# Performance work log

Measured on AMD Instinct MI355X. Metric: run time of the kernel, lower is better.

The kernel has to match this reference:

```python
import jax, jax.numpy as jnp
import numpy as np

N_EMBD = 768
HEAD_SIZE = 64
B, T = 8, 4096


def setup_inputs() -> dict:
    key = jax.random.key(0)
    ks = jax.random.split(key, 7)
    s = 0.02  # small init scale for weights
    return {
        "x": jax.random.normal(ks[0], (B, T, N_EMBD), dtype=jnp.float32),
        "Wq": jax.random.normal(ks[1], (N_EMBD, HEAD_SIZE), dtype=jnp.float32) * s,
        "bq": jax.random.normal(ks[2], (HEAD_SIZE,), dtype=jnp.float32) * s,
        "Wk": jax.random.normal(ks[3], (N_EMBD, HEAD_SIZE), dtype=jnp.float32) * s,
        "bk": jax.random.normal(ks[4], (HEAD_SIZE,), dtype=jnp.float32) * s,
        "Wv": jax.random.normal(ks[5], (N_EMBD, HEAD_SIZE), dtype=jnp.float32) * s,
        "bv": jax.random.normal(ks[6], (HEAD_SIZE,), dtype=jnp.float32) * s,
    }


def reference(x, Wq, bq, Wk, bk, Wv, bv):
    # x: [B, T, C]; note: scale uses C = n_embd (input dim), per the original code.
    C = x.shape[-1]
    scale = jnp.asarray(C, x.dtype) ** -0.5
    q = x @ Wq + bq  # [B, T, H]
    k = x @ Wk + bk  # [B, T, H]
    v = x @ Wv + bv  # [B, T, H]
    wei = jnp.einsum("bqh,bkh->bqk", q, k) * scale  # [B, T, T]
    att = jax.nn.softmax(wei, axis=-1)
    # dropout p=0.0 (eval mode) -> identity
    out = jnp.einsum("bqk,bkh->bqh", att, v)  # [B, T, H]
    return out
```

## Files before the change

### kernel.cpp

```cpp
#include <hip/hip_runtime.h>
#include <stdint.h>

#define T_SEQ 4096
#define CEMB 768
#define HS 64

typedef __attribute__((ext_vector_type(8))) short bf16x8;
typedef __attribute__((ext_vector_type(16))) float f32x16;
typedef __attribute__((ext_vector_type(4))) unsigned int u32x4;

__device__ __forceinline__ short bfru(float f) {
    uint32_t u = __builtin_bit_cast(uint32_t, f);
    return (short)((u + 0x8000u) >> 16);
}
__device__ __forceinline__ uint32_t cvtpk_bf16(float lo, float hi) {
    uint32_t r;
    asm("v_cvt_pk_bf16_f32 %0, %1, %2" : "=v"(r) : "v"(lo), "v"(hi));
    return r;
}

#define QSCALE (0.036084391824351615f * 1.4426950408889634f)

__global__ __launch_bounds__(256) void prep_wt(const float* __restrict__ Wq,
                                               const float* __restrict__ Wk,
                                               const float* __restrict__ Wv,
                                               short* __restrict__ wtf) {
    const int p = blockIdx.x;
    const int tid = threadIdx.x;
    const int lane = tid & 63, jp = tid >> 6;
    const int l31 = lane & 31, lhi = lane >> 5;
    const int kq = p % 48, ct = p / 48;
    const int k = kq * 16 + lhi * 8 + jp * 2;
    const int nn = ct * 32 + l31;
    const float* W = nn < 64 ? Wq : (nn < 128 ? Wk : Wv);
    const int col = nn & 63;
    uint32_t lo = (uint16_t)bfru(W[k * 64 + col]);
    uint32_t hi = (uint16_t)bfru(W[(k + 1) * 64 + col]);
    *(uint32_t*)&wtf[(p * 64 + lane) * 8 + jp * 2] = lo | (hi << 16);
}

__global__ __launch_bounds__(256, 2) void qkv_proj(const float* __restrict__ x,
        const float* __restrict__ bq, const float* __restrict__ bk, const float* __restrict__ bv,
        const short* __restrict__ wtf,
        short* __restrict__ qo, short* __restrict__ ko, short* __restrict__ vto) {
    __shared__ short S[2][64 * 72];

    const int tid  = threadIdx.x;
    const int wave = tid >> 6, lane = tid & 63;
    const int l31  = lane & 31, lhi = lane >> 5;
    const int rg   = wave & 1;
    const int ctb  = (wave >> 1) * 3;
    const int rowbase = blockIdx.x * 64;

    f32x16 acc[3];
    #pragma unroll
    for (int c = 0; c < 3; ++c) {
        const int ct = ctb + c, nn = ct * 32 + l31;
        const float bb = nn < 64 ? bq[nn] : (nn < 128 ? bk[nn - 64] : bv[nn - 128]);
        #pragma unroll
        for (int r = 0; r < 16; ++r) acc[c][r] = bb;
    }

    const int sr = tid >> 2, sseg = (tid & 3) * 16;
    const float* xrow = x + (long)(rowbase + sr) * CEMB + sseg;
    const short* wfb = wtf + (long)ctb * 48 * 512 + lane * 8;

    float4 RA0, RA1, RA2, RA3;
    float4 RB0, RB1, RB2, RB3;
    {
        const float4* s0 = (const float4*)xrow;
        RA0 = s0[0]; RA1 = s0[1]; RA2 = s0[2]; RA3 = s0[3];
        const float4* s1 = (const float4*)(xrow + 64);
        RB0 = s1[0]; RB1 = s1[1]; RB2 = s1[2]; RB3 = s1[3];
        bf16x8 w0, w1;
        w0[0]=bfru(RA0.x); w0[1]=bfru(RA0.y); w0[2]=bfru(RA0.z); w0[3]=bfru(RA0.w);
        w0[4]=bfru(RA1.x); w0[5]=bfru(RA1.y); w0[6]=bfru(RA1.z); w0[7]=bfru(RA1.w);
        w1[0]=bfru(RA2.x); w1[1]=bfru(RA2.y); w1[2]=bfru(RA2.z); w1[3]=bfru(RA2.w);
        w1[4]=bfru(RA3.x); w1[5]=bfru(RA3.y); w1[6]=bfru(RA3.z); w1[7]=bfru(RA3.w);
        *(bf16x8*)&S[0][sr * 72 + sseg]     = w0;
        *(bf16x8*)&S[0][sr * 72 + sseg + 8] = w1;
    }
    __syncthreads();

    #pragma unroll
    for (int kt = 0; kt < 12; ++kt) {
        const int cur = kt & 1;
        bf16x8 wfr[12];
        #pragma unroll
        for (int kc = 0; kc < 4; ++kc)
            #pragma unroll
            for (int c = 0; c < 3; ++c)
                wfr[kc * 3 + c] = *(const bf16x8*)(wfb + ((c * 48 + kt * 4 + kc) << 9));
        if (kt + 2 < 12) {
            const float4* sn = (const float4*)(xrow + (kt + 2) * 64);
            if (cur == 0) { RA0 = sn[0]; RA1 = sn[1]; RA2 = sn[2]; RA3 = sn[3]; }
            else          { RB0 = sn[0]; RB1 = sn[1]; RB2 = sn[2]; RB3 = sn[3]; }
        }
        #pragma unroll
        for (int kc = 0; kc < 4; ++kc) {
            bf16x8 af = *(const bf16x8*)&S[cur][(rg * 32 + l31) * 72 + kc * 16 + lhi * 8];
            acc[0] = __builtin_amdgcn_mfma_f32_32x32x16_bf16(af, wfr[kc * 3 + 0], acc[0], 0, 0, 0);
            acc[1] = __builtin_amdgcn_mfma_f32_32x32x16_bf16(af, wfr[kc * 3 + 1], acc[1], 0, 0, 0);
            acc[2] = __builtin_amdgcn_mfma_f32_32x32x16_bf16(af, wfr[kc * 3 + 2], acc[2], 0, 0, 0);
        }
        if (kt + 1 < 12) {
            bf16x8 w0, w1;
            if (cur == 0) {
                w0[0]=bfru(RB0.x); w0[1]=bfru(RB0.y); w0[2]=bfru(RB0.z); w0[3]=bfru(RB0.w);
                w0[4]=bfru(RB1.x); w0[5]=bfru(RB1.y); w0[6]=bfru(RB1.z); w0[7]=bfru(RB1.w);
                w1[0]=bfru(RB2.x); w1[1]=bfru(RB2.y); w1[2]=bfru(RB2.z); w1[3]=bfru(RB2.w);
                w1[4]=bfru(RB3.x); w1[5]=bfru(RB3.y); w1[6]=bfru(RB3.z); w1[7]=bfru(RB3.w);
            } else {
                w0[0]=bfru(RA0.x); w0[1]=bfru(RA0.y); w0[2]=bfru(RA0.z); w0[3]=bfru(RA0.w);
                w0[4]=bfru(RA1.x); w0[5]=bfru(RA1.y); w0[6]=bfru(RA1.z); w0[7]=bfru(RA1.w);
                w1[0]=bfru(RA2.x); w1[1]=bfru(RA2.y); w1[2]=bfru(RA2.z); w1[3]=bfru(RA2.w);
                w1[4]=bfru(RA3.x); w1[5]=bfru(RA3.y); w1[6]=bfru(RA3.z); w1[7]=bfru(RA3.w);
            }
            *(bf16x8*)&S[cur ^ 1][sr * 72 + sseg]     = w0;
            *(bf16x8*)&S[cur ^ 1][sr * 72 + sseg + 8] = w1;
        }
        __syncthreads();
    }

    #pragma unroll
    for (int c = 0; c < 3; ++c) {
        const int ct = ctb + c;
        if (ct < 2) {
            #pragma unroll
            for (int r = 0; r < 16; ++r) {
                const int row = rg * 32 + (r & 3) + 8 * (r >> 2) + 4 * lhi;
                qo[(long)(rowbase + row) * HS + ct * 32 + l31] = bfru(acc[c][r] * QSCALE);
            }
        } else if (ct < 4) {
            #pragma unroll
            for (int r = 0; r < 16; ++r) {
                const int row = rg * 32 + (r & 3) + 8 * (r >> 2) + 4 * lhi;
                ko[(long)(rowbase + row) * HS + (ct - 2) * 32 + l31] = bfru(acc[c][r]);
            }
        } else {
            #pragma unroll
            for (int r = 0; r < 16; ++r) {
                const int row = rg * 32 + (r & 3) + 8 * (r >> 2) + 4 * lhi;
                S[0][((ct - 4) * 32 + l31) * 72 + row] = bfru(acc[c][r]);
            }
        }
    }
    __syncthreads();
    if (tid < 128) {
        const int vcol = tid >> 1, hh = tid & 1;
        const int b = rowbase >> 12, t0 = rowbase & 4095;
        short* dst = vto + ((long)b * HS + vcol) * T_SEQ + t0 + hh * 32;
        #pragma unroll
        for (int i = 0; i < 4; ++i)
            *(bf16x8*)(dst + i * 8) = *(const bf16x8*)&S[0][vcol * 72 + hh * 32 + i * 8];
    }
}

__global__ __launch_bounds__(256, 2) void attn(const short* __restrict__ qm,
        const short* __restrict__ km, const short* __restrict__ vtm,
        float* __restrict__ Op, float* __restrict__ lp, const int ks,
        float* __restrict__ outdirect) {
    __shared__ short Klds[2][64 * 72];
    __shared__ short Vlds[2][64 * 72];
    __shared__ float Lred[4][2][32];

    const int tid  = threadIdx.x;
    const int wave = tid >> 6, lane = tid & 63;
    const int l31  = lane & 31, lhi = lane >> 5;
    const int idx  = blockIdx.x;
    const int b = idx & 7, s = (idx >> 3) % ks, qt = idx / (8 * ks);
    const int slab = T_SEQ / ks, nkt = slab / 64;

    const short* qb = qm + ((long)b * T_SEQ + qt * 256 + wave * 64) * HS;
    const short* kb = km + ((long)b * T_SEQ + s * slab) * HS;
    const short* vb = vtm + (long)b * HS * T_SEQ + s * slab;

    bf16x8 qf[2][4];
    #pragma unroll
    for (int qs = 0; qs < 2; ++qs)
        #pragma unroll
        for (int kc = 0; kc < 4; ++kc)
            qf[qs][kc] = *(const bf16x8*)&qb[(qs * 32 + l31) * HS + kc * 16 + lhi * 8];

    f32x16 oacc[2][2] = {};
    float lsum[2] = {0.f, 0.f};

    const int sr = tid >> 2, sc = (tid & 3) * 16;
    const short* kp = kb + sr * HS + sc;
    const short* vp = vb + sr * T_SEQ + sc;

    bf16x8 kr0 = *(const bf16x8*)kp, kr1 = *(const bf16x8*)(kp + 8);
    bf16x8 vr0 = *(const bf16x8*)vp, vr1 = *(const bf16x8*)(vp + 8);
    *(bf16x8*)&Klds[0][sr * 72 + sc]     = kr0;
    *(bf16x8*)&Klds[0][sr * 72 + sc + 8] = kr1;
    *(bf16x8*)&Vlds[0][sr * 72 + sc]     = vr0;
    *(bf16x8*)&Vlds[0][sr * 72 + sc + 8] = vr1;
    __syncthreads();

    for (int kt = 0; kt < nkt; ++kt) {
        const int cur = kt & 1;
        const bool pfe = (kt + 1 < nkt);
        if (pfe) {
            const short* kp2 = kp + (kt + 1) * (64 * HS);
            const short* vp2 = vp + (kt + 1) * 64;
            kr0 = *(const bf16x8*)kp2; kr1 = *(const bf16x8*)(kp2 + 8);
            vr0 = *(const bf16x8*)vp2; vr1 = *(const bf16x8*)(vp2 + 8);
        }
        const short* Kc = Klds[cur];
        const short* Vc = Vlds[cur];
        #pragma unroll
        for (int ct = 0; ct < 2; ++ct) {
            const short* krow = &Kc[(ct * 32 + l31) * 72 + lhi * 8];
            bf16x8 kf0 = *(const bf16x8*)(krow);
            bf16x8 kf1 = *(const bf16x8*)(krow + 16);
            bf16x8 kf2 = *(const bf16x8*)(krow + 32);
            bf16x8 kf3 = *(const bf16x8*)(krow + 48);
            const short* vrow = &Vc[l31 * 72 + ct * 32 + lhi * 8];
            bf16x8 vf00 = *(const bf16x8*)(vrow);
            bf16x8 vf10 = *(const bf16x8*)(vrow + 16);
            bf16x8 vf01 = *(const bf16x8*)(vrow + 32 * 72);
            bf16x8 vf11 = *(const bf16x8*)(vrow + 32 * 72 + 16);
            #pragma unroll
            for (int qs = 0; qs < 2; ++qs) {
                f32x16 z = {};
                z = __builtin_amdgcn_mfma_f32_32x32x16_bf16(kf0, qf[qs][0], z, 0, 0, 0);
                z = __builtin_amdgcn_mfma_f32_32x32x16_bf16(kf1, qf[qs][1], z, 0, 0, 0);
                z = __builtin_amdgcn_mfma_f32_32x32x16_bf16(kf2, qf[qs][2], z, 0, 0, 0);
                z = __builtin_amdgcn_mfma_f32_32x32x16_bf16(kf3, qf[qs][3], z, 0, 0, 0);
                #pragma unroll
                for (int r = 0; r < 16; ++r) z[r] = __builtin_amdgcn_exp2f(z[r]);
                lsum[qs] += (((z[0]+z[1])+(z[2]+z[3])) + ((z[4]+z[5])+(z[6]+z[7])))
                          + (((z[8]+z[9])+(z[10]+z[11])) + ((z[12]+z[13])+(z[14]+z[15])));
                uint32_t x0 = cvtpk_bf16(z[0],  z[1]),  y0 = cvtpk_bf16(z[4],  z[5]);
                uint32_t x1 = cvtpk_bf16(z[2],  z[3]),  y1 = cvtpk_bf16(z[6],  z[7]);
                uint32_t x2 = cvtpk_bf16(z[8],  z[9]),  y2 = cvtpk_bf16(z[12], z[13]);
                uint32_t x3 = cvtpk_bf16(z[10], z[11]), y3 = cvtpk_bf16(z[14], z[15]);
                asm("v_permlane32_swap_b32 %0, %1" : "+v"(x0), "+v"(y0));
                asm("v_permlane32_swap_b32 %0, %1" : "+v"(x1), "+v"(y1));
                asm("v_permlane32_swap_b32 %0, %1" : "+v"(x2), "+v"(y2));
                asm("v_permlane32_swap_b32 %0, %1" : "+v"(x3), "+v"(y3));
                u32x4 t0 = {x0, x1, y0, y1};
                u32x4 t1 = {x2, x3, y2, y3};
                bf16x8 pa0 = __builtin_bit_cast(bf16x8, t0);
                bf16x8 pa1 = __builtin_bit_cast(bf16x8, t1);
                oacc[qs][0] = __builtin_amdgcn_mfma_f32_32x32x16_bf16(pa0, vf00, oacc[qs][0], 0, 0, 0);
                oacc[qs][1] = __builtin_amdgcn_mfma_f32_32x32x16_bf16(pa0, vf01, oacc[qs][1], 0, 0, 0);
                oacc[qs][0] = __builtin_amdgcn_mfma_f32_32x32x16_bf16(pa1, vf10, oacc[qs][0], 0, 0, 0);
                oacc[qs][1] = __builtin_amdgcn_mfma_f32_32x32x16_bf16(pa1, vf11, oacc[qs][1], 0, 0, 0);
            }
        }
        if (pfe) {
            const int nxt = cur ^ 1;
            *(bf16x8*)&Klds[nxt][sr * 72 + sc]     = kr0;
            *(bf16x8*)&Klds[nxt][sr * 72 + sc + 8] = kr1;
            *(bf16x8*)&Vlds[nxt][sr * 72 + sc]     = vr0;
            *(bf16x8*)&Vlds[nxt][sr * 72 + sc + 8] = vr1;
        }
        __syncthreads();
    }

    #pragma unroll
    for (int qs = 0; qs < 2; ++qs) lsum[qs] += __shfl_xor(lsum[qs], 32);

    const long rowg = (long)b * T_SEQ + qt * 256 + wave * 64;
    if (outdirect) {
        if (lhi == 0) { Lred[wave][0][l31] = lsum[0]; Lred[wave][1][l31] = lsum[1]; }
        __syncthreads();
        float* ob = outdirect + rowg * HS;
        #pragma unroll
        for (int qs = 0; qs < 2; ++qs)
            #pragma unroll
            for (int ht = 0; ht < 2; ++ht)
                #pragma unroll
                for (int r = 0; r < 16; ++r) {
                    const int row = (r & 3) + 8 * (r >> 2) + 4 * lhi;
                    ob[(long)(qs * 32 + row) * HS + ht * 32 + l31] =
                        oacc[qs][ht][r] / Lred[wave][qs][row];
                }
    } else {
        float* op = Op + ((long)s * 32768 + rowg) * HS;
        #pragma unroll
        for (int qs = 0; qs < 2; ++qs)
            #pragma unroll
            for (int ht = 0; ht < 2; ++ht)
                #pragma unroll
                for (int r = 0; r < 16; ++r) {
                    const int row = (r & 3) + 8 * (r >> 2) + 4 * lhi;
                    op[(qs * 32 + row) * HS + ht * 32 + l31] = oacc[qs][ht][r];
                }
        if (lhi == 0) {
            lp[(long)s * 32768 + rowg + l31]      = lsum[0];
            lp[(long)s * 32768 + rowg + 32 + l31] = lsum[1];
        }
    }
}

__global__ __launch_bounds__(256) void combine(const float4* __restrict__ Op,
        const float* __restrict__ lp, float4* __restrict__ out, const int ks) {
    const int idx = blockIdx.x * 256 + threadIdx.x;
    const int row = idx >> 4, h4 = idx & 15;
    float ox = 0.f, oy = 0.f, oz = 0.f, ow = 0.f, l = 0.f;
    for (int s = 0; s < ks; ++s) {
        float4 t = Op[(long)(s * 32768 + row) * 16 + h4];
        ox += t.x; oy += t.y; oz += t.z; ow += t.w;
        l += lp[s * 32768 + row];
    }
    const float inv = 1.0f / l;
    float4 o; o.x = ox * inv; o.y = oy * inv; o.z = oz * inv; o.w = ow * inv;
    out[(long)row * 16 + h4] = o;
}

extern "C" void kernel_launch(void* const* d_in, const int* in_sizes, int n_in,
                              void* d_out, int out_size, void* d_ws, size_t ws_size,
                              hipStream_t stream) {
    const float* x  = (const float*)d_in[0];
    const float* Wq = (const float*)d_in[1];
    const float* bq = (const float*)d_in[2];
    const float* Wk = (const float*)d_in[3];
    const float* bk = (const float*)d_in[4];
    const float* Wv = (const float*)d_in[5];
    const float* bv = (const float*)d_in[6];

    char* ws = (char*)d_ws;
    short* qo  = (short*)(ws);
    short* ko  = (short*)(ws + (4u << 20));
    short* vto = (short*)(ws + (8u << 20));
    short* wtf = (short*)(ws + (12u << 20));
    const size_t opOff = 12582912u + 294912u;
    float* Op = (float*)(ws + opOff);

    const size_t per_s = 8388608u + 131072u;
    int ks = (ws_size >= opOff + 4 * per_s) ? 4
           : (ws_size >= opOff + 2 * per_s) ? 2 : 1;
    float* lp = (float*)(ws + opOff + (size_t)ks * 8388608u);

    prep_wt<<<288, 256, 0, stream>>>(Wq, Wk, Wv, wtf);
    qkv_proj<<<512, 256, 0, stream>>>(x, bq, bk, bv, wtf, qo, ko, vto);
    attn<<<128 * ks, 256, 0, stream>>>(qo, ko, vto, Op, lp, ks,
                                       ks == 1 ? (float*)d_out : nullptr);
    if (ks > 1)
        combine<<<2048, 256, 0, stream>>>((const float4*)Op, lp, (float4*)d_out, ks);
}
```

Before: 216.2 us.

## Fuse weight prep, QKV projection, attention and combine into one persistent kernel

Replaces four separate kernel launches with a single 512-block kernel whose stages are separated by software grid barriers built on atomic counters in workspace, which are zeroed by a memset before each launch. The aim is to remove launch gaps and per-kernel tail effects between the small stages. The risks are deadlock if all 512 blocks cannot be co-resident, the cost of spinning on global atomics, and the grid being fixed at 512 blocks, which leaves blocks idle in stages that need fewer.

After: 398.6 us. 1.84x slower.

```diff
diff --git a/kernel.cpp b/kernel.cpp
--- a/kernel.cpp
+++ b/kernel.cpp
@@ -4,6 +4,7 @@
 #define T_SEQ 4096
 #define CEMB 768
 #define HS 64
+#define GRIDN 512u
 
 typedef __attribute__((ext_vector_type(8))) short bf16x8;
 typedef __attribute__((ext_vector_type(16))) float f32x16;
@@ -21,293 +22,315 @@
 
 #define QSCALE (0.036084391824351615f * 1.4426950408889634f)
 
-__global__ __launch_bounds__(256) void prep_wt(const float* __restrict__ Wq,
-                                               const float* __restrict__ Wk,
-                                               const float* __restrict__ Wv,
-                                               short* __restrict__ wtf) {
-    const int p = blockIdx.x;
-    const int tid = threadIdx.x;
-    const int lane = tid & 63, jp = tid >> 6;
-    const int l31 = lane & 31, lhi = lane >> 5;
-    const int kq = p % 48, ct = p / 48;
-    const int k = kq * 16 + lhi * 8 + jp * 2;
-    const int nn = ct * 32 + l31;
-    const float* W = nn < 64 ? Wq : (nn < 128 ? Wk : Wv);
-    const int col = nn & 63;
-    uint32_t lo = (uint16_t)bfru(W[k * 64 + col]);
-    uint32_t hi = (uint16_t)bfru(W[(k + 1) * 64 + col]);
-    *(uint32_t*)&wtf[(p * 64 + lane) * 8 + jp * 2] = lo | (hi << 16);
-}
-
-__global__ __launch_bounds__(256, 2) void qkv_proj(const float* __restrict__ x,
-        const float* __restrict__ bq, const float* __restrict__ bk, const float* __restrict__ bv,
-        const short* __restrict__ wtf,
-        short* __restrict__ qo, short* __restrict__ ko, short* __restrict__ vto) {
-    __shared__ short S[2][64 * 72];
+__device__ __forceinline__ void gridbar(unsigned* c) {
+    __syncthreads();
+    if (threadIdx.x == 0) {
+        __hip_atomic_fetch_add(c, 1u, __ATOMIC_RELEASE, __HIP_MEMORY_SCOPE_AGENT);
+        while (__hip_atomic_load(c, __ATOMIC_ACQUIRE, __HIP_MEMORY_SCOPE_AGENT) < GRIDN)
+            __builtin_amdgcn_s_sleep(2);
+    }
+    __syncthreads();
+}
+
+__global__ __launch_bounds__(256, 2) void fused(
+        const float* __restrict__ x,
+        const float* __restrict__ Wq, const float* __restrict__ bq,
+        const float* __restrict__ Wk, const float* __restrict__ bk,
+        const float* __restrict__ Wv, const float* __restrict__ bv,
+        short* __restrict__ qo, short* __restrict__ ko, short* __restrict__ vto,
+        short* __restrict__ wtf, float* __restrict__ Op, float* __restrict__ lp,
+        unsigned* bars, const int ks, float* __restrict__ outf) {
+    __shared__ __align__(16) char smem[37888];
 
     const int tid  = threadIdx.x;
+    const int bid  = blockIdx.x;
     const int wave = tid >> 6, lane = tid & 63;
     const int l31  = lane & 31, lhi = lane >> 5;
-    const int rg   = wave & 1;
-    const int ctb  = (wave >> 1) * 3;
-    const int rowbase = blockIdx.x * 64;
-
-    f32x16 acc[3];
-    #pragma unroll
-    for (int c = 0; c < 3; ++c) {
-        const int ct = ctb + c, nn = ct * 32 + l31;
-        const float bb = nn < 64 ? bq[nn] : (nn < 128 ? bk[nn - 64] : bv[nn - 128]);
-        #pragma unroll
-        for (int r = 0; r < 16; ++r) acc[c][r] = bb;
-    }
-
-    const int sr = tid >> 2, sseg = (tid & 3) * 16;
-    const float* xrow = x + (long)(rowbase + sr) * CEMB + sseg;
-    const short* wfb = wtf + (long)ctb * 48 * 512 + lane * 8;
-
-    float4 RA0, RA1, RA2, RA3;
-    float4 RB0, RB1, RB2, RB3;
+
+    if (bid < 288) {
+        const int p = bid;
+        const int jp = wave;
+        const int kq = p % 48, ct = p / 48;
+        const int k = kq * 16 + lhi * 8 + jp * 2;
+        const int nn = ct * 32 + l31;
+        const float* W = nn < 64 ? Wq : (nn < 128 ? Wk : Wv);
+        const int col = nn & 63;
+        uint32_t lo = (uint16_t)bfru(W[k * 64 + col]);
+        uint32_t hi = (uint16_t)bfru(W[(k + 1) * 64 + col]);
+        *(uint32_t*)&wtf[(p * 64 + lane) * 8 + jp * 2] = lo | (hi << 16);
+    }
+    gridbar(bars + 0);
+
     {
-        const float4* s0 = (const float4*)xrow;
-        RA0 = s0[0]; RA1 = s0[1]; RA2 = s0[2]; RA3 = s0[3];
-        const float4* s1 = (const float4*)(xrow + 64);
-        RB0 = s1[0]; RB1 = s1[1]; RB2 = s1[2]; RB3 = s1[3];
-        bf16x8 w0, w1;
-        w0[0]=bfru(RA0.x); w0[1]=bfru(RA0.y); w0[2]=bfru(RA0.z); w0[3]=bfru(RA0.w);
-        w0[4]=bfru(RA1.x); w0[5]=bfru(RA1.y); w0[6]=bfru(RA1.z); w0[7]=bfru(RA1.w);
-        w1[0]=bfru(RA2.x); w1[1]=bfru(RA2.y); w1[2]=bfru(RA2.z); w1[3]=bfru(RA2.w);
-        w1[4]=bfru(RA3.x); w1[5]=bfru(RA3.y); w1[6]=bfru(RA3.z); w1[7]=bfru(RA3.w);
-        *(bf16x8*)&S[0][sr * 72 + sseg]     = w0;
-        *(bf16x8*)&S[0][sr * 72 + sseg + 8] = w1;
-    }
-    __syncthreads();
-
-    #pragma unroll
-    for (int kt = 0; kt < 12; ++kt) {
-        const int cur = kt & 1;
-        bf16x8 wfr[12];
-        #pragma unroll
-        for (int kc = 0; kc < 4; ++kc)
-            #pragma unroll
-            for (int c = 0; c < 3; ++c)
-                wfr[kc * 3 + c] = *(const bf16x8*)(wfb + ((c * 48 + kt * 4 + kc) << 9));
-        if (kt + 2 < 12) {
-            const float4* sn = (const float4*)(xrow + (kt + 2) * 64);
-            if (cur == 0) { RA0 = sn[0]; RA1 = sn[1]; RA2 = sn[2]; RA3 = sn[3]; }
-            else          { RB0 = sn[0]; RB1 = sn[1]; RB2 = sn[2]; RB3 = sn[3]; }
-        }
-        #pragma unroll
-        for (int kc = 0; kc < 4; ++kc) {
-            bf16x8 af = *(const bf16x8*)&S[cur][(rg * 32 + l31) * 72 + kc * 16 + lhi * 8];
-            acc[0] = __builtin_amdgcn_mfma_f32_32x32x16_bf16(af, wfr[kc * 3 + 0], acc[0], 0, 0, 0);
-            acc[1] = __builtin_amdgcn_mfma_f32_32x32x16_bf16(af, wfr[kc * 3 + 1], acc[1], 0, 0, 0);
-            acc[2] = __builtin_amdgcn_mfma_f32_32x32x16_bf16(af, wfr[kc * 3 + 2], acc[2], 0, 0, 0);
-        }
-        if (kt + 1 < 12) {
+        short* S0 = (short*)smem;
+        short* S1 = (short*)(smem + 9216);
+        const int rg   = wave & 1;
+        const int ctb  = (wave >> 1) * 3;
+        const int rowbase = bid * 64;
+
+        f32x16 acc[3];
+        #pragma unroll
+        for (int c = 0; c < 3; ++c) {
+            const int ct = ctb + c, nn = ct * 32 + l31;
+            const float bb = nn < 64 ? bq[nn] : (nn < 128 ? bk[nn - 64] : bv[nn - 128]);
+            #pragma unroll
+            for (int r = 0; r < 16; ++r) acc[c][r] = bb;
+        }
+
+        const int sr = tid >> 2, sseg = (tid & 3) * 16;
+        const float* xrow = x + (long)(rowbase + sr) * CEMB + sseg;
+        const short* wfb = wtf + (long)ctb * 48 * 512 + lane * 8;
+
+        float4 RA0, RA1, RA2, RA3;
+        float4 RB0, RB1, RB2, RB3;
+        {
+            const float4* s0 = (const float4*)xrow;
+            RA0 = s0[0]; RA1 = s0[1]; RA2 = s0[2]; RA3 = s0[3];
+            const float4* s1 = (const float4*)(xrow + 64);
+            RB0 = s1[0]; RB1 = s1[1]; RB2 = s1[2]; RB3 = s1[3];
             bf16x8 w0, w1;
-            if (cur == 0) {
-                w0[0]=bfru(RB0.x); w0[1]=bfru(RB0.y); w0[2]=bfru(RB0.z); w0[3]=bfru(RB0.w);
-                w0[4]=bfru(RB1.x); w0[5]=bfru(RB1.y); w0[6]=bfru(RB1.z); w0[7]=bfru(RB1.w);
-                w1[0]=bfru(RB2.x); w1[1]=bfru(RB2.y); w1[2]=bfru(RB2.z); w1[3]=bfru(RB2.w);
-                w1[4]=bfru(RB3.x); w1[5]=bfru(RB3.y); w1[6]=bfru(RB3.z); w1[7]=bfru(RB3.w);
+            w0[0]=bfru(RA0.x); w0[1]=bfru(RA0.y); w0[2]=bfru(RA0.z); w0[3]=bfru(RA0.w);
+            w0[4]=bfru(RA1.x); w0[5]=bfru(RA1.y); w0[6]=bfru(RA1.z); w0[7]=bfru(RA1.w);
+            w1[0]=bfru(RA2.x); w1[1]=bfru(RA2.y); w1[2]=bfru(RA2.z); w1[3]=bfru(RA2.w);
+            w1[4]=bfru(RA3.x); w1[5]=bfru(RA3.y); w1[6]=bfru(RA3.z); w1[7]=bfru(RA3.w);
+            *(bf16x8*)&S0[sr * 72 + sseg]     = w0;
+            *(bf16x8*)&S0[sr * 72 + sseg + 8] = w1;
+        }
+        __syncthreads();
+
+        #pragma unroll
+        for (int kt = 0; kt < 12; ++kt) {
+            const int cur = kt & 1;
+            short* Sc = cur ? S1 : S0;
+            short* Sn = cur ? S0 : S1;
+            bf16x8 wfr[12];
+            #pragma unroll
+            for (int kc = 0; kc < 4; ++kc)
+                #pragma unroll
+                for (int c = 0; c < 3; ++c)
+                    wfr[kc * 3 + c] = *(const bf16x8*)(wfb + ((c * 48 + kt * 4 + kc) << 9));
+            if (kt + 2 < 12) {
+                const float4* sn = (const float4*)(xrow + (kt + 2) * 64);
+                if (cur == 0) { RA0 = sn[0]; RA1 = sn[1]; RA2 = sn[2]; RA3 = sn[3]; }
+                else          { RB0 = sn[0]; RB1 = sn[1]; RB2 = sn[2]; RB3 = sn[3]; }
+            }
+            #pragma unroll
+            for (int kc = 0; kc < 4; ++kc) {
+                bf16x8 af = *(const bf16x8*)&Sc[(rg * 32 + l31) * 72 + kc * 16 + lhi * 8];
+                acc[0] = __builtin_amdgcn_mfma_f32_32x32x16_bf16(af, wfr[kc * 3 + 0], acc[0], 0, 0, 0);
+                acc[1] = __builtin_amdgcn_mfma_f32_32x32x16_bf16(af, wfr[kc * 3 + 1], acc[1], 0, 0, 0);
+                acc[2] = __builtin_amdgcn_mfma_f32_32x32x16_bf16(af, wfr[kc * 3 + 2], acc[2], 0, 0, 0);
+            }
+            if (kt + 1 < 12) {
+                bf16x8 w0, w1;
+                if (cur == 0) {
+                    w0[0]=bfru(RB0.x); w0[1]=bfru(RB0.y); w0[2]=bfru(RB0.z); w0[3]=bfru(RB0.w);
+                    w0[4]=bfru(RB1.x); w0[5]=bfru(RB1.y); w0[6]=bfru(RB1.z); w0[7]=bfru(RB1.w);
+                    w1[0]=bfru(RB2.x); w1[1]=bfru(RB2.y); w1[2]=bfru(RB2.z); w1[3]=bfru(RB2.w);
+                    w1[4]=bfru(RB3.x); w1[5]=bfru(RB3.y); w1[6]=bfru(RB3.z); w1[7]=bfru(RB3.w);
+                } else {
+                    w0[0]=bfru(RA0.x); w0[1]=bfru(RA0.y); w0[2]=bfru(RA0.z); w0[3]=bfru(RA0.w);
+                    w0[4]=bfru(RA1.x); w0[5]=bfru(RA1.y); w0[6]=bfru(RA1.z); w0[7]=bfru(RA1.w);
+                    w1[0]=bfru(RA2.x); w1[1]=bfru(RA2.y); w1[2]=bfru(RA2.z); w1[3]=bfru(RA2.w);
+                    w1[4]=bfru(RA3.x); w1[5]=bfru(RA3.y); w1[6]=bfru(RA3.z); w1[7]=bfru(RA3.w);
+                }
+                *(bf16x8*)&Sn[sr * 72 + sseg]     = w0;
+                *(bf16x8*)&Sn[sr * 72 + sseg + 8] = w1;
+            }
+            __syncthreads();
+        }
+
+        #pragma unroll
+        for (int c = 0; c < 3; ++c) {
+            const int ct = ctb + c;
+            if (ct < 2) {
+                #pragma unroll
+                for (int r = 0; r < 16; ++r) {
+                    const int row = rg * 32 + (r & 3) + 8 * (r >> 2) + 4 * lhi;
+                    qo[(long)(rowbase + row) * HS + ct * 32 + l31] = bfru(acc[c][r] * QSCALE);
+                }
+            } else if (ct < 4) {
+                #pragma unroll
+                for (int r = 0; r < 16; ++r) {
+                    const int row = rg * 32 + (r & 3) + 8 * (r >> 2) + 4 * lhi;
+                    ko[(long)(rowbase + row) * HS + (ct - 2) * 32 + l31] = bfru(acc[c][r]);
+                }
             } else {
-                w0[0]=bfru(RA0.x); w0[1]=bfru(RA0.y); w0[2]=bfru(RA0.z); w0[3]=bfru(RA0.w);
-                w0[4]=bfru(RA1.x); w0[5]=bfru(RA1.y); w0[6]=bfru(RA1.z); w0[7]=bfru(RA1.w);
-                w1[0]=bfru(RA2.x); w1[1]=bfru(RA2.y); w1[2]=bfru(RA2.z); w1[3]=bfru(RA2.w);
-                w1[4]=bfru(RA3.x); w1[5]=bfru(RA3.y); w1[6]=bfru(RA3.z); w1[7]=bfru(RA3.w);
-            }
-            *(bf16x8*)&S[cur ^ 1][sr * 72 + sseg]     = w0;
-            *(bf16x8*)&S[cur ^ 1][sr * 72 + sseg + 8] = w1;
+                #pragma unroll
+                for (int r = 0; r < 16; ++r) {
+                    const int row = rg * 32 + (r & 3) + 8 * (r >> 2) + 4 * lhi;
+                    S0[((ct - 4) * 32 + l31) * 72 + row] = bfru(acc[c][r]);
+                }
+            }
         }
         __syncthreads();
-    }
-
-    #pragma unroll
-    for (int c = 0; c < 3; ++c) {
-        const int ct = ctb + c;
-        if (ct < 2) {
-            #pragma unroll
-            for (int r = 0; r < 16; ++r) {
-                const int row = rg * 32 + (r & 3) + 8 * (r >> 2) + 4 * lhi;
-                qo[(long)(rowbase + row) * HS + ct * 32 + l31] = bfru(acc[c][r] * QSCALE);
-            }
-        } else if (ct < 4) {
-            #pragma unroll
-            for (int r = 0; r < 16; ++r) {
-                const int row = rg * 32 + (r & 3) + 8 * (r >> 2) + 4 * lhi;
-                ko[(long)(rowbase + row) * HS + (ct - 2) * 32 + l31] = bfru(acc[c][r]);
-            }
+        if (tid < 128) {
+            const int vcol = tid >> 1, hh = tid & 1;
+            const int b = rowbase >> 12, t0 = rowbase & 4095;
+            short* dst = vto + ((long)b * HS + vcol) * T_SEQ + t0 + hh * 32;
+            #pragma unroll
+            for (int i = 0; i < 4; ++i)
+                *(bf16x8*)(dst + i * 8) = *(const bf16x8*)&S0[vcol * 72 + hh * 32 + i * 8];
+        }
+    }
+    gridbar(bars + 1);
+
+    if (bid < 128 * ks) {
+        short* KldsB = (short*)smem;
+        short* VldsB = (short*)(smem + 18432);
+        float* LredB = (float*)(smem + 36864);
+
+        const int idx = bid;
+        const int b = idx & 7, s = (idx >> 3) % ks, qt = idx / (8 * ks);
+        const int slab = T_SEQ / ks, nkt = slab / 64;
+
+        const short* qb = qo + ((long)b * T_SEQ + qt * 256 + wave * 64) * HS;
+        const short* kb = ko + ((long)b * T_SEQ + s * slab) * HS;
+        const short* vb = vto + (long)b * HS * T_SEQ + s * slab;
+
+        bf16x8 qf[2][4];
+        #pragma unroll
+        for (int qs = 0; qs < 2; ++qs)
+            #pragma unroll
+            for (int kc = 0; kc < 4; ++kc)
+                qf[qs][kc] = *(const bf16x8*)&qb[(qs * 32 + l31) * HS + kc * 16 + lhi * 8];
+
+        f32x16 oacc[2][2] = {};
+        float lsum[2] = {0.f, 0.f};
+
+        const int sr = tid >> 2, sc = (tid & 3) * 16;
+        const short* kp = kb + sr * HS + sc;
+        const short* vp = vb + sr * T_SEQ + sc;
+
+        bf16x8 kr0 = *(const bf16x8*)kp, kr1 = *(const bf16x8*)(kp + 8);
+        bf16x8 vr0 = *(const bf16x8*)vp, vr1 = *(const bf16x8*)(vp + 8);
+        *(bf16x8*)&KldsB[sr * 72 + sc]     = kr0;
+        *(bf16x8*)&KldsB[sr * 72 + sc + 8] = kr1;
+        *(bf16x8*)&VldsB[sr * 72 + sc]     = vr0;
+        *(bf16x8*)&VldsB[sr * 72 + sc + 8] = vr1;
+        __syncthreads();
+
+        for (int kt = 0; kt < nkt; ++kt) {
+            const int cur = kt & 1;
+            const bool pfe = (kt + 1 < nkt);
+            if (pfe) {
+                const short* kp2 = kp + (kt + 1) * (64 * HS);
+                const short* vp2 = vp + (kt + 1) * 64;
+                kr0 = *(const bf16x8*)kp2; kr1 = *(const bf16x8*)(kp2 + 8);
+                vr0 = *(const bf16x8*)vp2; vr1 = *(const bf16x8*)(vp2 + 8);
+            }
+            const short* Kc = KldsB + cur * 4608;
+            const short* Vc = VldsB + cur * 4608;
+            #pragma unroll
+            for (int ct = 0; ct < 2; ++ct) {
+                const short* krow = &Kc[(ct * 32 + l31) * 72 + lhi * 8];
+                bf16x8 kf0 = *(const bf16x8*)(krow);
+                bf16x8 kf1 = *(const bf16x8*)(krow + 16);
+                bf16x8 kf2 = *(const bf16x8*)(krow + 32);
+                bf16x8 kf3 = *(const bf16x8*)(krow + 48);
+                const short* vrow = &Vc[l31 * 72 + ct * 32 + lhi * 8];
+                bf16x8 vf00 = *(const bf16x8*)(vrow);
+                bf16x8 vf10 = *(const bf16x8*)(vrow + 16);
+                bf16x8 vf01 = *(const bf16x8*)(vrow + 32 * 72);
+                bf16x8 vf11 = *(const bf16x8*)(vrow + 32 * 72 + 16);
+                #pragma unroll
+                for (int qs = 0; qs < 2; ++qs) {
+                    f32x16 z = {};
+                    z = __builtin_amdgcn_mfma_f32_32x32x16_bf16(kf0, qf[qs][0], z, 0, 0, 0);
+                    z = __builtin_amdgcn_mfma_f32_32x32x16_bf16(kf1, qf[qs][1], z, 0, 0, 0);
+                    z = __builtin_amdgcn_mfma_f32_32x32x16_bf16(kf2, qf[qs][2], z, 0, 0, 0);
+                    z = __builtin_amdgcn_mfma_f32_32x32x16_bf16(kf3, qf[qs][3], z, 0, 0, 0);
+                    #pragma unroll
+                    for (int r = 0; r < 16; ++r) z[r] = __builtin_amdgcn_exp2f(z[r]);
+                    lsum[qs] += (((z[0]+z[1])+(z[2]+z[3])) + ((z[4]+z[5])+(z[6]+z[7])))
+                              + (((z[8]+z[9])+(z[10]+z[11])) + ((z[12]+z[13])+(z[14]+z[15])));
+                    uint32_t x0 = cvtpk_bf16(z[0],  z[1]),  y0 = cvtpk_bf16(z[4],  z[5]);
+                    uint32_t x1 = cvtpk_bf16(z[2],  z[3]),  y1 = cvtpk_bf16(z[6],  z[7]);
+                    uint32_t x2 = cvtpk_bf16(z[8],  z[9]),  y2 = cvtpk_bf16(z[12], z[13]);
+                    uint32_t x3 = cvtpk_bf16(z[10], z[11]), y3 = cvtpk_bf16(z[14], z[15]);
+                    asm("v_permlane32_swap_b32 %0, %1" : "+v"(x0), "+v"(y0));
+                    asm("v_permlane32_swap_b32 %0, %1" : "+v"(x1), "+v"(y1));
+                    asm("v_permlane32_swap_b32 %0, %1" : "+v"(x2), "+v"(y2));
+                    asm("v_permlane32_swap_b32 %0, %1" : "+v"(x3), "+v"(y3));
+                    u32x4 t0 = {x0, x1, y0, y1};
+                    u32x4 t1 = {x2, x3, y2, y3};
+                    bf16x8 pa0 = __builtin_bit_cast(bf16x8, t0);
+                    bf16x8 pa1 = __builtin_bit_cast(bf16x8, t1);
+                    oacc[qs][0] = __builtin_amdgcn_mfma_f32_32x32x16_bf16(pa0, vf00, oacc[qs][0], 0, 0, 0);
+                    oacc[qs][1] = __builtin_amdgcn_mfma_f32_32x32x16_bf16(pa0, vf01, oacc[qs][1], 0, 0, 0);
+                    oacc[qs][0] = __builtin_amdgcn_mfma_f32_32x32x16_bf16(pa1, vf10, oacc[qs][0], 0, 0, 0);
+                    oacc[qs][1] = __builtin_amdgcn_mfma_f32_32x32x16_bf16(pa1, vf11, oacc[qs][1], 0, 0, 0);
+                }
+            }
+            if (pfe) {
+                short* Kn = KldsB + (cur ^ 1) * 4608;
+                short* Vn = VldsB + (cur ^ 1) * 4608;
+                *(bf16x8*)&Kn[sr * 72 + sc]     = kr0;
+                *(bf16x8*)&Kn[sr * 72 + sc + 8] = kr1;
+                *(bf16x8*)&Vn[sr * 72 + sc]     = vr0;
+                *(bf16x8*)&Vn[sr * 72 + sc + 8] = vr1;
+            }
+            __syncthreads();
+        }
+
+        #pragma unroll
+        for (int qs = 0; qs < 2; ++qs) lsum[qs] += __shfl_xor(lsum[qs], 32);
+
+        const long rowg = (long)b * T_SEQ + qt * 256 + wave * 64;
+        if (ks == 1) {
+            if (lhi == 0) {
+                LredB[(wave * 2 + 0) * 32 + l31] = lsum[0];
+                LredB[(wave * 2 + 1) * 32 + l31] = lsum[1];
+            }
+            __syncthreads();
+            float* ob = outf + rowg * HS;
+            #pragma unroll
+            for (int qs = 0; qs < 2; ++qs)
+                #pragma unroll
+                for (int ht = 0; ht < 2; ++ht)
+                    #pragma unroll
+                    for (int r = 0; r < 16; ++r) {
+                        const int row = (r & 3) + 8 * (r >> 2) + 4 * lhi;
+                        ob[(long)(qs * 32 + row) * HS + ht * 32 + l31] =
+                            oacc[qs][ht][r] / LredB[(wave * 2 + qs) * 32 + row];
+                    }
         } else {
-            #pragma unroll
-            for (int r = 0; r < 16; ++r) {
-                const int row = rg * 32 + (r & 3) + 8 * (r >> 2) + 4 * lhi;
-                S[0][((ct - 4) * 32 + l31) * 72 + row] = bfru(acc[c][r]);
-            }
-        }
-    }
-    __syncthreads();
-    if (tid < 128) {
-        const int vcol = tid >> 1, hh = tid & 1;
-        const int b = rowbase >> 12, t0 = rowbase & 4095;
-        short* dst = vto + ((long)b * HS + vcol) * T_SEQ + t0 + hh * 32;
-        #pragma unroll
-        for (int i = 0; i < 4; ++i)
-            *(bf16x8*)(dst + i * 8) = *(const bf16x8*)&S[0][vcol * 72 + hh * 32 + i * 8];
-    }
-}
-
-__global__ __launch_bounds__(256, 2) void attn(const short* __restrict__ qm,
-        const short* __restrict__ km, const short* __restrict__ vtm,
-        float* __restrict__ Op, float* __restrict__ lp, const int ks,
-        float* __restrict__ outdirect) {
-    __shared__ short Klds[2][64 * 72];
-    __shared__ short Vlds[2][64 * 72];
-    __shared__ float Lred[4][2][32];
-
-    const int tid  = threadIdx.x;
-    const int wave = tid >> 6, lane = tid & 63;
-    const int l31  = lane & 31, lhi = lane >> 5;
-    const int idx  = blockIdx.x;
-    const int b = idx & 7, s = (idx >> 3) % ks, qt = idx / (8 * ks);
-    const int slab = T_SEQ / ks, nkt = slab / 64;
-
-    const short* qb = qm + ((long)b * T_SEQ + qt * 256 + wave * 64) * HS;
-    const short* kb = km + ((long)b * T_SEQ + s * slab) * HS;
-    const short* vb = vtm + (long)b * HS * T_SEQ + s * slab;
-
-    bf16x8 qf[2][4];
-    #pragma unroll
-    for (int qs = 0; qs < 2; ++qs)
-        #pragma unroll
-        for (int kc = 0; kc < 4; ++kc)
-            qf[qs][kc] = *(const bf16x8*)&qb[(qs * 32 + l31) * HS + kc * 16 + lhi * 8];
-
-    f32x16 oacc[2][2] = {};
-    float lsum[2] = {0.f, 0.f};
-
-    const int sr = tid >> 2, sc = (tid & 3) * 16;
-    const short* kp = kb + sr * HS + sc;
-    const short* vp = vb + sr * T_SEQ + sc;
-
-    bf16x8 kr0 = *(const bf16x8*)kp, kr1 = *(const bf16x8*)(kp + 8);
-    bf16x8 vr0 = *(const bf16x8*)vp, vr1 = *(const bf16x8*)(vp + 8);
-    *(bf16x8*)&Klds[0][sr * 72 + sc]     = kr0;
-    *(bf16x8*)&Klds[0][sr * 72 + sc + 8] = kr1;
-    *(bf16x8*)&Vlds[0][sr * 72 + sc]     = vr0;
-    *(bf16x8*)&Vlds[0][sr * 72 + sc + 8] = vr1;
-    __syncthreads();
-
-    for (int kt = 0; kt < nkt; ++kt) {
-        const int cur = kt & 1;
-        const bool pfe = (kt + 1 < nkt);
-        if (pfe) {
-            const short* kp2 = kp + (kt + 1) * (64 * HS);
-            const short* vp2 = vp + (kt + 1) * 64;
-            kr0 = *(const bf16x8*)kp2; kr1 = *(const bf16x8*)(kp2 + 8);
-            vr0 = *(const bf16x8*)vp2; vr1 = *(const bf16x8*)(vp2 + 8);
-        }
-        const short* Kc = Klds[cur];
-        const short* Vc = Vlds[cur];
-        #pragma unroll
-        for (int ct = 0; ct < 2; ++ct) {
-            const short* krow = &Kc[(ct * 32 + l31) * 72 + lhi * 8];
-            bf16x8 kf0 = *(const bf16x8*)(krow);
-            bf16x8 kf1 = *(const bf16x8*)(krow + 16);
-            bf16x8 kf2 = *(const bf16x8*)(krow + 32);
-            bf16x8 kf3 = *(const bf16x8*)(krow + 48);
-            const short* vrow = &Vc[l31 * 72 + ct * 32 + lhi * 8];
-            bf16x8 vf00 = *(const bf16x8*)(vrow);
-            bf16x8 vf10 = *(const bf16x8*)(vrow + 16);
-            bf16x8 vf01 = *(const bf16x8*)(vrow + 32 * 72);
-            bf16x8 vf11 = *(const bf16x8*)(vrow + 32 * 72 + 16);
-            #pragma unroll
-            for (int qs = 0; qs < 2; ++qs) {
-                f32x16 z = {};
-                z = __builtin_amdgcn_mfma_f32_32x32x16_bf16(kf0, qf[qs][0], z, 0, 0, 0);
-                z = __builtin_amdgcn_mfma_f32_32x32x16_bf16(kf1, qf[qs][1], z, 0, 0, 0);
-                z = __builtin_amdgcn_mfma_f32_32x32x16_bf16(kf2, qf[qs][2], z, 0, 0, 0);
-                z = __builtin_amdgcn_mfma_f32_32x32x16_bf16(kf3, qf[qs][3], z, 0, 0, 0);
-                #pragma unroll
-                for (int r = 0; r < 16; ++r) z[r] = __builtin_amdgcn_exp2f(z[r]);
-                lsum[qs] += (((z[0]+z[1])+(z[2]+z[3])) + ((z[4]+z[5])+(z[6]+z[7])))
-                          + (((z[8]+z[9])+(z[10]+z[11])) + ((z[12]+z[13])+(z[14]+z[15])));
-                uint32_t x0 = cvtpk_bf16(z[0],  z[1]),  y0 = cvtpk_bf16(z[4],  z[5]);
-                uint32_t x1 = cvtpk_bf16(z[2],  z[3]),  y1 = cvtpk_bf16(z[6],  z[7]);
-                uint32_t x2 = cvtpk_bf16(z[8],  z[9]),  y2 = cvtpk_bf16(z[12], z[13]);
-                uint32_t x3 = cvtpk_bf16(z[10], z[11]), y3 = cvtpk_bf16(z[14], z[15]);
-                asm("v_permlane32_swap_b32 %0, %1" : "+v"(x0), "+v"(y0));
-                asm("v_permlane32_swap_b32 %0, %1" : "+v"(x1), "+v"(y1));
-                asm("v_permlane32_swap_b32 %0, %1" : "+v"(x2), "+v"(y2));
-                asm("v_permlane32_swap_b32 %0, %1" : "+v"(x3), "+v"(y3));
-                u32x4 t0 = {x0, x1, y0, y1};
-                u32x4 t1 = {x2, x3, y2, y3};
-                bf16x8 pa0 = __builtin_bit_cast(bf16x8, t0);
-                bf16x8 pa1 = __builtin_bit_cast(bf16x8, t1);
-                oacc[qs][0] = __builtin_amdgcn_mfma_f32_32x32x16_bf16(pa0, vf00, oacc[qs][0], 0, 0, 0);
-                oacc[qs][1] = __builtin_amdgcn_mfma_f32_32x32x16_bf16(pa0, vf01, oacc[qs][1], 0, 0, 0);
-                oacc[qs][0] = __builtin_amdgcn_mfma_f32_32x32x16_bf16(pa1, vf10, oacc[qs][0], 0, 0, 0);
-                oacc[qs][1] = __builtin_amdgcn_mfma_f32_32x32x16_bf16(pa1, vf11, oacc[qs][1], 0, 0, 0);
-            }
-        }
-        if (pfe) {
-            const int nxt = cur ^ 1;
-            *(bf16x8*)&Klds[nxt][sr * 72 + sc]     = kr0;
-            *(bf16x8*)&Klds[nxt][sr * 72 + sc + 8] = kr1;
-            *(bf16x8*)&Vlds[nxt][sr * 72 + sc]     = vr0;
-            *(bf16x8*)&Vlds[nxt][sr * 72 + sc + 8] = vr1;
-        }
-        __syncthreads();
-    }
-
-    #pragma unroll
-    for (int qs = 0; qs < 2; ++qs) lsum[qs] += __shfl_xor(lsum[qs], 32);
-
-    const long rowg = (long)b * T_SEQ + qt * 256 + wave * 64;
-    if (outdirect) {
-        if (lhi == 0) { Lred[wave][0][l31] = lsum[0]; Lred[wave][1][l31] = lsum[1]; }
-        __syncthreads();
-        float* ob = outdirect + rowg * HS;
-        #pragma unroll
-        for (int qs = 0; qs < 2; ++qs)
-            #pragma unroll
-            for (int ht = 0; ht < 2; ++ht)
-                #pragma unroll
-                for (int r = 0; r < 16; ++r) {
-                    const int row = (r & 3) + 8 * (r >> 2) + 4 * lhi;
-                    ob[(long)(qs * 32 + row) * HS + ht * 32 + l31] =
-                        oacc[qs][ht][r] / Lred[wave][qs][row];
-                }
-    } else {
-        float* op = Op + ((long)s * 32768 + rowg) * HS;
-        #pragma unroll
-        for (int qs = 0; qs < 2; ++qs)
-            #pragma unroll
-            for (int ht = 0; ht < 2; ++ht)
-                #pragma unroll
-                for (int r = 0; r < 16; ++r) {
-                    const int row = (r & 3) + 8 * (r >> 2) + 4 * lhi;
-                    op[(qs * 32 + row) * HS + ht * 32 + l31] = oacc[qs][ht][r];
-                }
-        if (lhi == 0) {
-            lp[(long)s * 32768 + rowg + l31]      = lsum[0];
-            lp[(long)s * 32768 + rowg + 32 + l31] = lsum[1];
-        }
-    }
-}
-
-__global__ __launch_bounds__(256) void combine(const float4* __restrict__ Op,
-        const float* __restrict__ lp, float4* __restrict__ out, const int ks) {
-    const int idx = blockIdx.x * 256 + threadIdx.x;
-    const int row = idx >> 4, h4 = idx & 15;
-    float ox = 0.f, oy = 0.f, oz = 0.f, ow = 0.f, l = 0.f;
-    for (int s = 0; s < ks; ++s) {
-        float4 t = Op[(long)(s * 32768 + row) * 16 + h4];
-        ox += t.x; oy += t.y; oz += t.z; ow += t.w;
-        l += lp[s * 32768 + row];
-    }
-    const float inv = 1.0f / l;
-    float4 o; o.x = ox * inv; o.y = oy * inv; o.z = oz * inv; o.w = ow * inv;
-    out[(long)row * 16 + h4] = o;
+            float* op = Op + ((long)s * 32768 + rowg) * HS;
+            #pragma unroll
+            for (int qs = 0; qs < 2; ++qs)
+                #pragma unroll
+                for (int ht = 0; ht < 2; ++ht)
+                    #pragma unroll
+                    for (int r = 0; r < 16; ++r) {
+                        const int row = (r & 3) + 8 * (r >> 2) + 4 * lhi;
+                        op[(qs * 32 + row) * HS + ht * 32 + l31] = oacc[qs][ht][r];
+                    }
+            if (lhi == 0) {
+                lp[(long)s * 32768 + rowg + l31]      = lsum[0];
+                lp[(long)s * 32768 + rowg + 32 + l31] = lsum[1];
+            }
+        }
+    }
+
+    if (ks > 1) {
+        gridbar(bars + 2);
+        const float4* Opv = (const float4*)Op;
+        float4* outv = (float4*)outf;
+        #pragma unroll
+        for (int i = 0; i < 4; ++i) {
+            const int idx = (bid * 4 + i) * 256 + tid;
+            const int row = idx >> 4, h4 = idx & 15;
+            float ox = 0.f, oy = 0.f, oz = 0.f, ow = 0.f, l = 0.f;
+            for (int s2 = 0; s2 < ks; ++s2) {
+                float4 t = Opv[(long)(s2 * 32768 + row) * 16 + h4];
+                ox += t.x; oy += t.y; oz += t.z; ow += t.w;
+                l += lp[s2 * 32768 + row];
+            }
+            const float inv = 1.0f / l;
+            float4 o; o.x = ox * inv; o.y = oy * inv; o.z = oz * inv; o.w = ow * inv;
+            outv[(long)row * 16 + h4] = o;
+        }
+    }
 }
 
 extern "C" void kernel_launch(void* const* d_in, const int* in_sizes, int n_in,
@@ -326,18 +349,18 @@
     short* ko  = (short*)(ws + (4u << 20));
     short* vto = (short*)(ws + (8u << 20));
     short* wtf = (short*)(ws + (12u << 20));
-    const size_t opOff = 12582912u + 294912u;
+    const size_t barOff = 12582912u + 294912u;
+    const size_t opOff  = barOff + 1024u;
     float* Op = (float*)(ws + opOff);
 
     const size_t per_s = 8388608u + 131072u;
     int ks = (ws_size >= opOff + 4 * per_s) ? 4
            : (ws_size >= opOff + 2 * per_s) ? 2 : 1;
     float* lp = (float*)(ws + opOff + (size_t)ks * 8388608u);
-
-    prep_wt<<<288, 256, 0, stream>>>(Wq, Wk, Wv, wtf);
-    qkv_proj<<<512, 256, 0, stream>>>(x, bq, bk, bv, wtf, qo, ko, vto);
-    attn<<<128 * ks, 256, 0, stream>>>(qo, ko, vto, Op, lp, ks,
-                                       ks == 1 ? (float*)d_out : nullptr);
-    if (ks > 1)
-        combine<<<2048, 256, 0, stream>>>((const float4*)Op, lp, (float4*)d_out, ks);
-}
+    unsigned* bars = (unsigned*)(ws + barOff);
+
+    hipMemsetAsync(ws + barOff, 0, 1024, stream);
+    fused<<<GRIDN, 256, 0, stream>>>(x, Wq, bq, Wk, bk, Wv, bv,
+                                     qo, ko, vto, wtf, Op, lp, bars, ks,
+                                     (float*)d_out);
+}
```
